# Performance work log

Measured on AMD Instinct MI355X. Metric: run time of the kernel, lower is better.

## Reference

```python
import jax, jax.numpy as jnp
from jax import lax
import numpy as np

CHANNEL_N = 16
HIDDEN = 128
INPUT_CH = 1
KSIZE = 7
STEPS = 10
EPS = 1e-5


def setup_inputs() -> dict:
    key = jax.random.key(0)
    ks = jax.random.split(key, 8)
    B, H, W = 8, 256, 256
    x = jax.random.normal(ks[0], (B, H, W, CHANNEL_N), dtype=jnp.float32)
    # stochastic fire masks, one per step (torch: bernoulli_(p=fire_rate) under no_grad)
    masks = jax.random.bernoulli(ks[1], 0.5, (STEPS, B, 1, H, W))
    # depthwise conv: groups=channel_n -> weight [C,1,K,K]
    conv_w = jax.random.normal(ks[2], (CHANNEL_N, 1, KSIZE, KSIZE), dtype=jnp.float32) * 0.05
    conv_b = jax.random.normal(ks[3], (CHANNEL_N,), dtype=jnp.float32) * 0.05
    # fc0: 1x1 conv [hidden, 2*C]
    fc0_w = jax.random.normal(ks[4], (HIDDEN, 2 * CHANNEL_N), dtype=jnp.float32) * 0.1
    fc0_b = jax.random.normal(ks[5], (HIDDEN,), dtype=jnp.float32) * 0.05
    # fc1: 1x1 conv [C - input_channels, hidden], no bias (zero-init in torch; random here)
    fc1_w = jax.random.normal(ks[6], (CHANNEL_N - INPUT_CH, HIDDEN), dtype=jnp.float32) * 0.02
    bn_gamma = jnp.ones((HIDDEN,), dtype=jnp.float32)
    bn_beta = jnp.zeros((HIDDEN,), dtype=jnp.float32)
    return {"x": x, "masks": masks, "conv_w": conv_w, "conv_b": conv_b,
            "fc0_w": fc0_w, "fc0_b": fc0_b, "fc1_w": fc1_w,
            "bn_gamma": bn_gamma, "bn_beta": bn_beta}


def _nca_forward(x, masks, conv_w, conv_b, fc0_w, fc0_b, fc1_w, bn_gamma, bn_beta):
    state = jnp.transpose(x, (0, 3, 1, 2))  # b h w c -> b c h w
    const_in = state[:, :INPUT_CH]
    pad = (KSIZE - 1) // 2

    def step(state, mask):
        # depthwise 7x7 conv, reflect padding
        sp = jnp.pad(state, ((0, 0), (0, 0), (pad, pad), (pad, pad)), mode='reflect')
        d = lax.conv_general_dilated(
            sp, conv_w, window_strides=(1, 1), padding='VALID',
            dimension_numbers=('NCHW', 'OIHW', 'NCHW'),
            feature_group_count=CHANNEL_N)
        d = d + conv_b[None, :, None, None]
        cat = jnp.concatenate([state, d], axis=1)  # [B, 2C, H, W]
        # fc0 (1x1 conv)
        h = jnp.einsum('bchw,oc->bohw', cat, fc0_w) + fc0_b[None, :, None, None]
        # BatchNorm2d with batch statistics (track_running_stats=False)
        mean = jnp.mean(h, axis=(0, 2, 3), keepdims=True)
        var = jnp.var(h, axis=(0, 2, 3), keepdims=True)
        h = (h - mean) * lax.rsqrt(var + EPS)
        h = h * bn_gamma[None, :, None, None] + bn_beta[None, :, None, None]
        h = jax.nn.relu(h)
        # fc1 (1x1 conv, no bias)
        delta = jnp.einsum('bohw,ko->bkhw', h, fc1_w)  # [B, C-1, H, W]
        delta = delta * mask  # stochastic fire (broadcast over channels)
        new = state[:, INPUT_CH:] + delta
        return jnp.concatenate([const_in, new], axis=1), None

    state, _ = lax.scan(step, state, masks.astype(state.dtype))
    return jnp.transpose(state, (0, 2, 3, 1))  # b c h w -> b h w c


def reference(x, masks, conv_w, conv_b, fc0_w, fc0_b, fc1_w, bn_gamma, bn_beta):
    return _nca_forward(x, masks, conv_w, conv_b, fc0_w, fc0_b, fc1_w, bn_gamma, bn_beta)
```

## Files before the change

kernel.cpp:

```cpp
#include <hip/hip_runtime.h>

#define CH 16
#define HID 128
#define NB 8
#define NH 256
#define NW 256
#define NPX (NB*NH*NW)
#define NSTEP 10
#define STEPSTATS 1536
#define GPW 8
#define KPW 4
#define SLAB 1280

typedef __attribute__((ext_vector_type(8))) short short8v;
typedef __attribute__((ext_vector_type(4))) float f32x4;

__device__ __forceinline__ int refl(int i, int n){
    if (i < 0) i = -i;
    if (i >= n) i = 2*n - 2 - i;
    return i;
}

__device__ __forceinline__ unsigned short f2bf(float x){
    unsigned int u = __float_as_uint(x);
    u += 0x7FFFu + ((u >> 16) & 1u);
    return (unsigned short)(u >> 16);
}
__device__ __forceinline__ float bf2f(unsigned short h){
    return __uint_as_float(((unsigned int)h) << 16);
}

__global__ void k_repack(const float* __restrict__ cw, const float* __restrict__ f1,
                         const float* __restrict__ w0, float* __restrict__ wp,
                         unsigned short* __restrict__ b0h, unsigned short* __restrict__ b0l,
                         unsigned short* __restrict__ b1h, unsigned short* __restrict__ b1l){
    int t = blockIdx.x*256 + threadIdx.x;
    if (t < 49*16){ int tap = t >> 4, c = t & 15; wp[tap*16 + c] = cw[c*49 + tap]; }
    if (t < 4096){
        int n = t >> 9, l = (t >> 3) & 63, i = t & 7;
        int o = 16*n + (l & 15), k = ((l >> 4) << 3) + i;
        float v = w0[o*32 + k];
        unsigned short hi = f2bf(v);
        b0h[t] = hi;
        b0l[t] = f2bf(v - bf2f(hi));
    }
    if (t < 2048){
        int tk = t >> 9, l = (t >> 3) & 63, i = t & 7;
        int c = l & 15, k = tk*32 + ((l >> 4) << 3) + i;
        float v = (c >= 1) ? f1[(c-1)*HID + k] : 0.f;
        unsigned short hi = f2bf(v);
        b1h[t] = hi;
        b1l[t] = f2bf(v - bf2f(hi));
    }
}

__global__ void k_zero(float* __restrict__ p, int n){
    int t = blockIdx.x*256 + threadIdx.x;
    if (t < n) p[t] = 0.f;
}

struct Row { float4 e[4]; float4 o[4]; };

__device__ __forceinline__ void fma4(float4& a, float4 w, float4 v){
    a.x += w.x*v.x; a.y += w.y*v.y; a.z += w.z*v.z; a.w += w.w*v.w;
}
__device__ __forceinline__ void ldrow(Row& r, const float4* L, int row, int tx){
    #pragma unroll
    for (int k=0;k<4;++k){
        r.e[k] = L[(row*2+0)*20 + tx + k];
        r.o[k] = L[(row*2+1)*20 + tx + k];
    }
}

__global__ __launch_bounds__(256,3)
void k_conv(const float* __restrict__ st, const float* __restrict__ wp,
            const float* __restrict__ cb, float* __restrict__ dout){
    __shared__ float4 tile4[38*2*20];
    __shared__ float4 cw4s[49];
    const int b = blockIdx.z >> 2, cg = blockIdx.z & 3;
    const int y0 = blockIdx.y*32, x0 = blockIdx.x*32;
    const int t = threadIdx.x;
    const int tx = t & 15, ty = t >> 4;

    if (t < 49) cw4s[t] = *(const float4*)&wp[t*16 + cg*4];
    for (int i = t; i < 38*38; i += 256){
        int py = i / 38, px = i - py*38;
        int gy = refl(y0 + py - 3, NH);
        int gx = refl(x0 + px - 3, NW);
        float4 v = *(const float4*)&st[(((size_t)b*NH + gy)*NW + gx)*CH + cg*4];
        tile4[(py*2 + (px&1))*20 + (px>>1)] = v;
    }
    __syncthreads();

    const float4* L = tile4;
    float4 bias = *(const float4*)&cb[cg*4];
    float4 a00 = bias, a01 = bias, a10 = bias, a11 = bias;
    Row A, B;
    ldrow(A, L, 2*ty,   tx);
    ldrow(B, L, 2*ty+1, tx);

#define CSTEP(dy, RA, RB, LOADNEXT, NR) \
    { \
        _Pragma("unroll") \
        for (int dx = 0; dx < 7; ++dx){ \
            float4 w4 = cw4s[(dy)*7 + dx]; \
            float4 v00 = ((dx)&1)   ? RA.o[(dx)>>1]   : RA.e[(dx)>>1]; \
            float4 v01 = ((dx+1)&1) ? RA.o[(dx+1)>>1] : RA.e[(dx+1)>>1]; \
            float4 v10 = ((dx)&1)   ? RB.o[(dx)>>1]   : RB.e[(dx)>>1]; \
            float4 v11 = ((dx+1)&1) ? RB.o[(dx+1)>>1] : RB.e[(dx+1)>>1]; \
            fma4(a00,w4,v00); fma4(a01,w4,v01); fma4(a10,w4,v10); fma4(a11,w4,v11); \
        } \
        if (LOADNEXT) ldrow(RA, L, NR, tx); \
    }

    CSTEP(0, A, B, 1, 2*ty+2)
    CSTEP(1, B, A, 1, 2*ty+3)
    CSTEP(2, A, B, 1, 2*ty+4)
    CSTEP(3, B, A, 1, 2*ty+5)
    CSTEP(4, A, B, 1, 2*ty+6)
    CSTEP(5, B, A, 1, 2*ty+7)
    CSTEP(6, A, B, 0, 0)
#undef CSTEP

    const size_t pr = ((size_t)b*NH + (size_t)(y0 + 2*ty))*NW + (x0 + 2*tx);
    *(float4*)&dout[(pr)*CH + cg*4]        = a00;
    *(float4*)&dout[(pr+1)*CH + cg*4]      = a01;
    *(float4*)&dout[(pr+NW)*CH + cg*4]     = a10;
    *(float4*)&dout[(pr+NW+1)*CH + cg*4]   = a11;
}

__global__ __launch_bounds__(512)
void k_stats(const float* __restrict__ st, const float* __restrict__ dv,
             float* __restrict__ S){
    __shared__ float lds[8*SLAB];
    const int t = threadIdx.x, lane = t & 63, w = t >> 6;
    const int lo = lane & 15, hi = lane >> 4;
    float* slab = &lds[w*SLAB];
    const int gw = blockIdx.x*8 + w;

    short8v ones;
    {
        short ov = (lo == 0) ? (short)0x3F80 : (short)0;
        #pragma unroll
        for (int i=0;i<8;++i) ones[i] = ov;
    }
    f32x4 a00 = (f32x4){0.f,0.f,0.f,0.f};
    f32x4 a01 = a00, a11 = a00, s0 = a00, s1 = a00;

    const int lp = lane >> 3, lq = lane & 7;
    const float* lbase = (lq < 4) ? st : dv;
    const int lch = (lq & 3) * 4;
    const size_t p0 = (size_t)gw * (KPW*32);

    float4 v[4];
    #pragma unroll
    for (int j2=0;j2<4;++j2)
        v[j2] = *(const float4*)&lbase[(p0 + lp + 8*j2)*CH + lch];

    #pragma unroll
    for (int j=0;j<KPW;++j){
        #pragma unroll
        for (int j2=0;j2<4;++j2){
            int p = lp + 8*j2;
            *(float2*)&slab[p*34 + lq*4]     = make_float2(v[j2].x, v[j2].y);
            *(float2*)&slab[p*34 + lq*4 + 2] = make_float2(v[j2].z, v[j2].w);
        }
        if (j+1 < KPW){
            const size_t pn = p0 + (size_t)(j+1)*32;
            #pragma unroll
            for (int j2=0;j2<4;++j2)
                v[j2] = *(const float4*)&lbase[(pn + lp + 8*j2)*CH + lch];
        }
        short8v r0h, r0l, r1h, r1l;
        #pragma unroll
        for (int ct=0;ct<2;++ct){
            #pragma unroll
            for (int i=0;i<8;++i){
                float f = slab[(hi*8+i)*34 + ct*16 + lo];
                unsigned int u = __float_as_uint(f);
                unsigned short ah = (unsigned short)(u >> 16);
                float r = f - __uint_as_float(u & 0xFFFF0000u);
                unsigned short al = (unsigned short)(__float_as_uint(r) >> 16);
                if (ct==0){ r0h[i]=(short)ah; r0l[i]=(short)al; }
                else      { r1h[i]=(short)ah; r1l[i]=(short)al; }
            }
        }
        s0 = __builtin_amdgcn_mfma_f32_16x16x32_bf16(ones, r0h, s0, 0,0,0);
        s0 = __builtin_amdgcn_mfma_f32_16x16x32_bf16(ones, r0l, s0, 0,0,0);
        s1 = __builtin_amdgcn_mfma_f32_16x16x32_bf16(ones, r1h, s1, 0,0,0);
        s1 = __builtin_amdgcn_mfma_f32_16x16x32_bf16(ones, r1l, s1, 0,0,0);
        a00 = __builtin_amdgcn_mfma_f32_16x16x32_bf16(r0h, r0h, a00, 0,0,0);
        a00 = __builtin_amdgcn_mfma_f32_16x16x32_bf16(r0l, r0h, a00, 0,0,0);
        a00 = __builtin_amdgcn_mfma_f32_16x16x32_bf16(r0h, r0l, a00, 0,0,0);
        a11 = __builtin_amdgcn_mfma_f32_16x16x32_bf16(r1h, r1h, a11, 0,0,0);
        a11 = __builtin_amdgcn_mfma_f32_16x16x32_bf16(r1l, r1h, a11, 0,0,0);
        a11 = __builtin_amdgcn_mfma_f32_16x16x32_bf16(r1h, r1l, a11, 0,0,0);
        a01 = __builtin_amdgcn_mfma_f32_16x16x32_bf16(r0h, r1h, a01, 0,0,0);
        a01 = __builtin_amdgcn_mfma_f32_16x16x32_bf16(r0l, r1h, a01, 0,0,0);
        a01 = __builtin_amdgcn_mfma_f32_16x16x32_bf16(r0h, r1l, a01, 0,0,0);
    }

    float* red = lds;
    #pragma unroll
    for (int k=0;k<4;++k){
        red[t*20 + k]      = a00[k];
        red[t*20 + 4 + k]  = a01[k];
        red[t*20 + 8 + k]  = a11[k];
        red[t*20 + 12 + k] = s0[k];
        red[t*20 + 16 + k] = s1[k];
    }
    __syncthreads();
    if (w == 0){
        float tmp[20];
        #pragma unroll
        for (int k=0;k<20;++k){
            float s = 0.f;
            #pragma unroll
            for (int ww=0;ww<8;++ww) s += red[(lane + 64*ww)*20 + k];
            tmp[k] = s;
        }
        #pragma unroll
        for (int r=0;r<4;++r){
            atomicAdd(&S[(hi*4+r)*32 + lo],        tmp[r]);
            atomicAdd(&S[(hi*4+r)*32 + 16 + lo],   tmp[4+r]);
            atomicAdd(&S[(16+lo)*32 + hi*4 + r],   tmp[4+r]);
            atomicAdd(&S[(16+hi*4+r)*32 + 16+lo],  tmp[8+r]);
        }
        if (hi == 0){
            atomicAdd(&S[1024 + lo],      tmp[12]);
            atomicAdd(&S[1024 + 16 + lo], tmp[16]);
        }
    }
}

__global__ void k_finalize(const float* __restrict__ S,
                           const float* __restrict__ w0, const float* __restrict__ b0,
                           const float* __restrict__ gam, const float* __restrict__ bet,
                           float* __restrict__ sc, float* __restrict__ sh){
    int o = threadIdx.x;
    const float inv = 1.f / (float)NPX;
    float w[32];
    #pragma unroll
    for (int c=0;c<32;++c) w[c] = w0[o*32+c];
    const float* su = S + 1024;
    float m1 = 0.f;
    #pragma unroll
    for (int c=0;c<32;++c) m1 += w[c]*su[c];
    m1 *= inv;
    float q = 0.f;
    for (int i=0;i<32;++i){
        float ti = 0.f;
        #pragma unroll
        for (int j=0;j<32;++j) ti += S[i*32+j]*w[j];
        q += w[i]*ti;
    }
    q *= inv;
    float var = q - m1*m1;
    float rstd = rsqrtf(var + 1e-5f);
    float mean = m1 + b0[o];
    float scale = rstd * gam[o];
    sc[o] = scale;
    sh[o] = bet[o] + (b0[o] - mean)*scale;
}

__global__ __launch_bounds__(256)
void k_update(const float* __restrict__ st, const float* __restrict__ dv,
              const int* __restrict__ msk,
              const unsigned short* __restrict__ gb0h, const unsigned short* __restrict__ gb0l,
              const unsigned short* __restrict__ gb1h, const unsigned short* __restrict__ gb1l,
              const float* __restrict__ sc, const float* __restrict__ sh,
              float* __restrict__ out){
    __shared__ float hbuf[4*16*132];
    const int lane = threadIdx.x & 63, w = threadIdx.x >> 6;
    const int lo16 = lane & 15, qw = lane >> 4;
    float* hb = &hbuf[w*16*132];

    const short8v* p0h = (const short8v*)gb0h;
    const short8v* p0l = (const short8v*)gb0l;
    const short8v* p1h = (const short8v*)gb1h;
    const short8v* p1l = (const short8v*)gb1l;
    short8v B0h[8], B0l[8], B1h[4], B1l[4];
    #pragma unroll
    for (int n=0;n<8;++n){ B0h[n] = p0h[n*64 + lane]; B0l[n] = p0l[n*64 + lane]; }
    #pragma unroll
    for (int tt=0;tt<4;++tt){ B1h[tt] = p1h[tt*64 + lane]; B1l[tt] = p1l[tt*64 + lane]; }
    float scr[8], shr[8];
    #pragma unroll
    for (int n=0;n<8;++n){ scr[n] = sc[16*n + lo16]; shr[n] = sh[16*n + lo16]; }

    const int gw = blockIdx.x*4 + w;
    const float* abase = (qw < 2) ? st : dv;
    const int choff = (qw & 1)*8;

    for (int gi = 0; gi < GPW; ++gi){
        const size_t pg0 = ((size_t)gw*GPW + gi)*16;
        const float* ap = abase + (pg0 + lo16)*CH + choff;
        float4 v0 = *(const float4*)ap;
        float4 v1 = *(const float4*)(ap + 4);
        float av[8] = {v0.x,v0.y,v0.z,v0.w,v1.x,v1.y,v1.z,v1.w};
        short8v ah, al;
        #pragma unroll
        for (int i=0;i<8;++i){
            unsigned short hi = f2bf(av[i]);
            ah[i] = (short)hi;
            al[i] = (short)f2bf(av[i] - bf2f(hi));
        }
        f32x4 acc[8];
        #pragma unroll
        for (int n=0;n<8;++n) acc[n] = (f32x4){0.f,0.f,0.f,0.f};
        #pragma unroll
        for (int n=0;n<8;++n){
            acc[n] = __builtin_amdgcn_mfma_f32_16x16x32_bf16(ah, B0h[n], acc[n], 0,0,0);
            acc[n] = __builtin_amdgcn_mfma_f32_16x16x32_bf16(al, B0h[n], acc[n], 0,0,0);
            acc[n] = __builtin_amdgcn_mfma_f32_16x16x32_bf16(ah, B0l[n], acc[n], 0,0,0);
        }
        #pragma unroll
        for (int n=0;n<8;++n){
            #pragma unroll
            for (int r=0;r<4;++r){
                float hp = fmaxf(acc[n][r]*scr[n] + shr[n], 0.f);
                hb[(qw*4 + r)*132 + 16*n + lo16] = hp;
            }
        }
        f32x4 dacc = (f32x4){0.f,0.f,0.f,0.f};
        #pragma unroll
        for (int tt=0;tt<4;++tt){
            const float* rp = &hb[lo16*132 + qw*8 + 32*tt];
            float4 h0 = *(const float4*)rp;
            float4 h1 = *(const float4*)(rp + 4);
            float hv[8] = {h0.x,h0.y,h0.z,h0.w,h1.x,h1.y,h1.z,h1.w};
            short8v ah2, al2;
            #pragma unroll
            for (int i=0;i<8;++i){
                unsigned short hi = f2bf(hv[i]);
                ah2[i] = (short)hi;
                al2[i] = (short)f2bf(hv[i] - bf2f(hi));
            }
            dacc = __builtin_amdgcn_mfma_f32_16x16x32_bf16(ah2, B1h[tt], dacc, 0,0,0);
            dacc = __builtin_amdgcn_mfma_f32_16x16x32_bf16(al2, B1h[tt], dacc, 0,0,0);
            dacc = __builtin_amdgcn_mfma_f32_16x16x32_bf16(ah2, B1l[tt], dacc, 0,0,0);
        }
        #pragma unroll
        for (int r=0;r<4;++r){
            const size_t p = pg0 + qw*4 + r;
            float stv = st[p*CH + lo16];
            float m = (float)msk[p];
            out[p*CH + lo16] = stv + dacc[r]*m;
        }
    }
}

extern "C" void kernel_launch(void* const* d_in, const int* in_sizes, int n_in,
                              void* d_out, int out_size, void* d_ws, size_t ws_size,
                              hipStream_t stream){
    const float* x   = (const float*)d_in[0];
    const int*   mk  = (const int*)d_in[1];
    const float* cw  = (const float*)d_in[2];
    const float* cb  = (const float*)d_in[3];
    const float* w0  = (const float*)d_in[4];
    const float* b0  = (const float*)d_in[5];
    const float* f1  = (const float*)d_in[6];
    const float* gam = (const float*)d_in[7];
    const float* bet = (const float*)d_in[8];

    float* ws    = (float*)d_ws;
    float* dbuf  = ws;
    float* sbuf  = ws + (size_t)NPX*CH;
    float* stats = ws + (size_t)2*NPX*CH;
    float* wp    = stats + NSTEP*STEPSTATS;
    unsigned short* b0h = (unsigned short*)(wp + 800);
    unsigned short* b0l = b0h + 4096;
    unsigned short* b1h = b0l + 4096;
    unsigned short* b1l = b1h + 2048;

    k_repack<<<16,256,0,stream>>>(cw, f1, w0, wp, b0h, b0l, b1h, b1l);
    k_zero<<<(NSTEP*STEPSTATS+255)/256,256,0,stream>>>(stats, NSTEP*STEPSTATS);

    const float* cur = x;
    float* outp = (float*)d_out;
    for (int s=0;s<NSTEP;++s){
        float* S  = stats + (size_t)s*STEPSTATS;
        float* sc = S + 1056;
        float* sh = S + 1184;
        float* nxt = (s & 1) ? outp : sbuf;
        k_conv<<<dim3(NW/32,NH/32,NB*4),256,0,stream>>>(cur, wp, cb, dbuf);
        k_stats<<<512,512,0,stream>>>(cur, dbuf, S);
        k_finalize<<<1,128,0,stream>>>(S, w0, b0, gam, bet, sc, sh);
        k_update<<<NPX/16/4/GPW,256,0,stream>>>(cur, dbuf, mk + (size_t)s*NPX,
                                                b0h, b0l, b1h, b1l, sc, sh, nxt);
        cur = nxt;
    }
}
```

Before: 1.238 ms.

## Fold BN scale into fc1 weights, bias into MFMA accumulator, single-bf16 hidden

The BatchNorm scale is folded into per-step fc1 weights in k_finalize, and the shift (divided by scale) seeds the fc0 MFMA accumulator, so the update kernel applies only ReLU. The hidden activations are packed to bf16 with a hardware convert and fed to fc1 as a single MFMA per tile, instead of a hi/lo split with three MFMAs. Operand order is swapped so each lane writes a float4 of output channels, vectorising the store. This removes many MFMAs and scalar conversions but lowers fc1 precision to plain bf16, and the bias trick divides by scale, which breaks if gamma is zero.

```diff
diff --git a/kernel.cpp b/kernel.cpp
--- a/kernel.cpp
+++ b/kernel.cpp
@@ -7,7 +7,7 @@
 #define NW 256
 #define NPX (NB*NH*NW)
 #define NSTEP 10
-#define STEPSTATS 1536
+#define STEPSTATS 2240
 #define GPW 8
 #define KPW 4
 #define SLAB 1280
@@ -29,11 +29,15 @@
 __device__ __forceinline__ float bf2f(unsigned short h){
     return __uint_as_float(((unsigned int)h) << 16);
 }
-
-__global__ void k_repack(const float* __restrict__ cw, const float* __restrict__ f1,
-                         const float* __restrict__ w0, float* __restrict__ wp,
-                         unsigned short* __restrict__ b0h, unsigned short* __restrict__ b0l,
-                         unsigned short* __restrict__ b1h, unsigned short* __restrict__ b1l){
+__device__ __forceinline__ unsigned int cvtpk(float lo, float hi){
+    unsigned int r;
+    asm("v_cvt_pk_bf16_f32 %0, %1, %2" : "=v"(r) : "v"(lo), "v"(hi));
+    return r;
+}
+
+__global__ void k_repack(const float* __restrict__ cw, const float* __restrict__ w0,
+                         float* __restrict__ wp,
+                         unsigned short* __restrict__ b0h, unsigned short* __restrict__ b0l){
     int t = blockIdx.x*256 + threadIdx.x;
     if (t < 49*16){ int tap = t >> 4, c = t & 15; wp[tap*16 + c] = cw[c*49 + tap]; }
     if (t < 4096){
@@ -43,14 +47,6 @@
         unsigned short hi = f2bf(v);
         b0h[t] = hi;
         b0l[t] = f2bf(v - bf2f(hi));
-    }
-    if (t < 2048){
-        int tk = t >> 9, l = (t >> 3) & 63, i = t & 7;
-        int c = l & 15, k = tk*32 + ((l >> 4) << 3) + i;
-        float v = (c >= 1) ? f1[(c-1)*HID + k] : 0.f;
-        unsigned short hi = f2bf(v);
-        b1h[t] = hi;
-        b1l[t] = f2bf(v - bf2f(hi));
     }
 }
 
@@ -236,7 +232,7 @@
 __global__ void k_finalize(const float* __restrict__ S,
                            const float* __restrict__ w0, const float* __restrict__ b0,
                            const float* __restrict__ gam, const float* __restrict__ bet,
-                           float* __restrict__ sc, float* __restrict__ sh){
+                           const float* __restrict__ f1, float* __restrict__ Sout){
     int o = threadIdx.x;
     const float inv = 1.f / (float)NPX;
     float w[32];
@@ -259,34 +255,37 @@
     float rstd = rsqrtf(var + 1e-5f);
     float mean = m1 + b0[o];
     float scale = rstd * gam[o];
-    sc[o] = scale;
-    sh[o] = bet[o] + (b0[o] - mean)*scale;
+    Sout[1056 + o] = bet[o]/scale + b0[o] - mean;
+    unsigned short* f1sh = (unsigned short*)(Sout + 1184);
+    const int base = (o>>5)*512 + ((o>>3)&3)*128 + (o&7);
+    f1sh[base] = 0;
+    #pragma unroll
+    for (int c=1;c<16;++c)
+        f1sh[base + c*8] = f2bf(f1[(c-1)*HID + o] * scale);
 }
 
 __global__ __launch_bounds__(256)
 void k_update(const float* __restrict__ st, const float* __restrict__ dv,
               const int* __restrict__ msk,
               const unsigned short* __restrict__ gb0h, const unsigned short* __restrict__ gb0l,
-              const unsigned short* __restrict__ gb1h, const unsigned short* __restrict__ gb1l,
-              const float* __restrict__ sc, const float* __restrict__ sh,
-              float* __restrict__ out){
-    __shared__ float hbuf[4*16*132];
+              const float* __restrict__ Sstep, float* __restrict__ out){
+    __shared__ __align__(16) unsigned int hls[4*16*68];
     const int lane = threadIdx.x & 63, w = threadIdx.x >> 6;
     const int lo16 = lane & 15, qw = lane >> 4;
-    float* hb = &hbuf[w*16*132];
+    unsigned int* hb = &hls[w*16*68];
 
     const short8v* p0h = (const short8v*)gb0h;
     const short8v* p0l = (const short8v*)gb0l;
-    const short8v* p1h = (const short8v*)gb1h;
-    const short8v* p1l = (const short8v*)gb1l;
-    short8v B0h[8], B0l[8], B1h[4], B1l[4];
+    const short8v* p1h = (const short8v*)(Sstep + 1184);
+    short8v B0h[8], B0l[8], B1h[4];
     #pragma unroll
     for (int n=0;n<8;++n){ B0h[n] = p0h[n*64 + lane]; B0l[n] = p0l[n*64 + lane]; }
     #pragma unroll
-    for (int tt=0;tt<4;++tt){ B1h[tt] = p1h[tt*64 + lane]; B1l[tt] = p1l[tt*64 + lane]; }
-    float scr[8], shr[8];
-    #pragma unroll
-    for (int n=0;n<8;++n){ scr[n] = sc[16*n + lo16]; shr[n] = sh[16*n + lo16]; }
+    for (int tt=0;tt<4;++tt) B1h[tt] = p1h[tt*64 + lane];
+    const float* shb = Sstep + 1056;
+    float4 shbv[8];
+    #pragma unroll
+    for (int n=0;n<8;++n) shbv[n] = *(const float4*)&shb[16*n + 4*qw];
 
     const int gw = blockIdx.x*4 + w;
     const float* abase = (qw < 2) ? st : dv;
@@ -301,52 +300,43 @@
         short8v ah, al;
         #pragma unroll
         for (int i=0;i<8;++i){
-            unsigned short hi = f2bf(av[i]);
-            ah[i] = (short)hi;
-            al[i] = (short)f2bf(av[i] - bf2f(hi));
+            unsigned int u = __float_as_uint(av[i]);
+            ah[i] = (short)(unsigned short)(u >> 16);
+            float r = av[i] - __uint_as_float(u & 0xFFFF0000u);
+            al[i] = (short)(unsigned short)(__float_as_uint(r) >> 16);
         }
         f32x4 acc[8];
         #pragma unroll
-        for (int n=0;n<8;++n) acc[n] = (f32x4){0.f,0.f,0.f,0.f};
+        for (int n=0;n<8;++n)
+            acc[n] = (f32x4){shbv[n].x, shbv[n].y, shbv[n].z, shbv[n].w};
         #pragma unroll
         for (int n=0;n<8;++n){
-            acc[n] = __builtin_amdgcn_mfma_f32_16x16x32_bf16(ah, B0h[n], acc[n], 0,0,0);
-            acc[n] = __builtin_amdgcn_mfma_f32_16x16x32_bf16(al, B0h[n], acc[n], 0,0,0);
-            acc[n] = __builtin_amdgcn_mfma_f32_16x16x32_bf16(ah, B0l[n], acc[n], 0,0,0);
+            acc[n] = __builtin_amdgcn_mfma_f32_16x16x32_bf16(B0h[n], ah, acc[n], 0,0,0);
+            acc[n] = __builtin_amdgcn_mfma_f32_16x16x32_bf16(B0h[n], al, acc[n], 0,0,0);
+            acc[n] = __builtin_amdgcn_mfma_f32_16x16x32_bf16(B0l[n], ah, acc[n], 0,0,0);
         }
         #pragma unroll
         for (int n=0;n<8;++n){
-            #pragma unroll
-            for (int r=0;r<4;++r){
-                float hp = fmaxf(acc[n][r]*scr[n] + shr[n], 0.f);
-                hb[(qw*4 + r)*132 + 16*n + lo16] = hp;
-            }
+            float h0 = fmaxf(acc[n][0], 0.f), h1 = fmaxf(acc[n][1], 0.f);
+            float h2 = fmaxf(acc[n][2], 0.f), h3 = fmaxf(acc[n][3], 0.f);
+            unsigned int wa = cvtpk(h0, h1), wb = cvtpk(h2, h3);
+            *(uint2*)&hb[lo16*68 + 8*n + 2*qw] = make_uint2(wa, wb);
         }
         f32x4 dacc = (f32x4){0.f,0.f,0.f,0.f};
         #pragma unroll
         for (int tt=0;tt<4;++tt){
-            const float* rp = &hb[lo16*132 + qw*8 + 32*tt];
-            float4 h0 = *(const float4*)rp;
-            float4 h1 = *(const float4*)(rp + 4);
-            float hv[8] = {h0.x,h0.y,h0.z,h0.w,h1.x,h1.y,h1.z,h1.w};
-            short8v ah2, al2;
-            #pragma unroll
-            for (int i=0;i<8;++i){
-                unsigned short hi = f2bf(hv[i]);
-                ah2[i] = (short)hi;
-                al2[i] = (short)f2bf(hv[i] - bf2f(hi));
-            }
-            dacc = __builtin_amdgcn_mfma_f32_16x16x32_bf16(ah2, B1h[tt], dacc, 0,0,0);
-            dacc = __builtin_amdgcn_mfma_f32_16x16x32_bf16(al2, B1h[tt], dacc, 0,0,0);
-            dacc = __builtin_amdgcn_mfma_f32_16x16x32_bf16(ah2, B1l[tt], dacc, 0,0,0);
-        }
-        #pragma unroll
-        for (int r=0;r<4;++r){
-            const size_t p = pg0 + qw*4 + r;
-            float stv = st[p*CH + lo16];
-            float m = (float)msk[p];
-            out[p*CH + lo16] = stv + dacc[r]*m;
-        }
+            short8v ah2 = *(const short8v*)&hb[lo16*68 + 16*tt + 4*qw];
+            dacc = __builtin_amdgcn_mfma_f32_16x16x32_bf16(B1h[tt], ah2, dacc, 0,0,0);
+        }
+        const size_t p = pg0 + lo16;
+        float4 stv = *(const float4*)&st[p*CH + 4*qw];
+        const float m = (float)msk[p];
+        float4 ov;
+        ov.x = stv.x + dacc[0]*m;
+        ov.y = stv.y + dacc[1]*m;
+        ov.z = stv.z + dacc[2]*m;
+        ov.w = stv.w + dacc[3]*m;
+        *(float4*)&out[p*CH + 4*qw] = ov;
     }
 }
 
@@ -370,24 +360,20 @@
     float* wp    = stats + NSTEP*STEPSTATS;
     unsigned short* b0h = (unsigned short*)(wp + 800);
     unsigned short* b0l = b0h + 4096;
-    unsigned short* b1h = b0l + 4096;
-    unsigned short* b1l = b1h + 2048;
-
-    k_repack<<<16,256,0,stream>>>(cw, f1, w0, wp, b0h, b0l, b1h, b1l);
+
+    k_repack<<<16,256,0,stream>>>(cw, w0, wp, b0h, b0l);
     k_zero<<<(NSTEP*STEPSTATS+255)/256,256,0,stream>>>(stats, NSTEP*STEPSTATS);
 
     const float* cur = x;
     float* outp = (float*)d_out;
     for (int s=0;s<NSTEP;++s){
-        float* S  = stats + (size_t)s*STEPSTATS;
-        float* sc = S + 1056;
-        float* sh = S + 1184;
+        float* S = stats + (size_t)s*STEPSTATS;
         float* nxt = (s & 1) ? outp : sbuf;
         k_conv<<<dim3(NW/32,NH/32,NB*4),256,0,stream>>>(cur, wp, cb, dbuf);
         k_stats<<<512,512,0,stream>>>(cur, dbuf, S);
-        k_finalize<<<1,128,0,stream>>>(S, w0, b0, gam, bet, sc, sh);
+        k_finalize<<<1,128,0,stream>>>(S, w0, b0, gam, bet, f1, S);
         k_update<<<NPX/16/4/GPW,256,0,stream>>>(cur, dbuf, mk + (size_t)s*NPX,
-                                                b0h, b0l, b1h, b1l, sc, sh, nxt);
+                                                b0h, b0l, S, nxt);
         cur = nxt;
     }
 }
```

Result: faster. 1.085 ms (-12.3%).
